# Optimization experiments

Measured on AMD Instinct MI355X. Metric: run time of the kernel, lower is better.

The kernel has to match this reference:

```python
import jax, jax.numpy as jnp
import numpy as np

BN_EPS = 1e-5


def _gin_layer(x, src, dst, W, b, num_nodes):
    # GINConv with eps=0: h_i = MLP(x_i + sum_{j in N(i)} x_j)
    agg = jax.ops.segment_sum(x[src], dst, num_segments=num_nodes)  # [N, F]
    h = (x + agg) @ W + b
    return jax.nn.relu(h)


def _batchnorm(h, gamma, beta):
    # training-mode BatchNorm1d: biased batch stats over the node dim
    mean = jnp.mean(h, axis=0)
    var = jnp.mean(jnp.square(h - mean), axis=0)
    return (h - mean) * jax.lax.rsqrt(var + BN_EPS) * gamma + beta


def setup_inputs() -> dict:
    key = jax.random.key(0)
    N, E, F, H = 50000, 800000, 128, 128
    ks = jax.random.split(key, 6)
    x = jax.random.normal(ks[0], (N, F), dtype=jnp.float32)
    edge_index = jax.random.randint(ks[1], (2, E), 0, N, dtype=jnp.int64)
    W1 = jax.random.normal(ks[2], (F, H), dtype=jnp.float32) * 0.05
    b1 = jnp.zeros((H,), dtype=jnp.float32)
    W2 = jax.random.normal(ks[3], (H, H), dtype=jnp.float32) * 0.05
    b2 = jnp.zeros((H,), dtype=jnp.float32)
    g1 = jnp.ones((H,), dtype=jnp.float32)
    be1 = jnp.zeros((H,), dtype=jnp.float32)
    g2 = jnp.ones((H,), dtype=jnp.float32)
    be2 = jnp.zeros((H,), dtype=jnp.float32)
    return {"x": x, "edge_index": edge_index, "W1": W1, "b1": b1,
            "W2": W2, "b2": b2, "g1": g1, "be1": be1, "g2": g2, "be2": be2}


def reference(x, edge_index, W1, b1, W2, b2, g1, be1, g2, be2):
    N = x.shape[0]
    src, dst = edge_index[0], edge_index[1]
    h = _gin_layer(x, src, dst, W1, b1, N)
    h = _batchnorm(h, g1, be1)
    h = _gin_layer(h, src, dst, W2, b2, N)
    return _batchnorm(h, g2, be2)
```

## Files before the change

### kernel.cpp

```cpp
#include <hip/hip_runtime.h>
#include <hip/hip_fp16.h>

#define FDIM 128
#define NGRP 8
#define CAP  64

typedef _Float16 half8_t __attribute__((ext_vector_type(8)));
typedef _Float16 half4_t __attribute__((ext_vector_type(4)));
typedef float float4_t __attribute__((ext_vector_type(4)));


__global__ void prep_kernel(int* __restrict__ zbase, int zn,
                            const float* __restrict__ x, _Float16* __restrict__ xh, int n4x,
                            const float* __restrict__ W1, _Float16* __restrict__ Wf1,
                            const float* __restrict__ W2, _Float16* __restrict__ Wf2,
                            int nzb, int ncb) {
  int b = blockIdx.x, t = threadIdx.x;
  if (b < nzb) {
    int i = b * 256 + t;
    if (i < zn) zbase[i] = 0;
  } else if (b < nzb + ncb) {
    int i = (b - nzb) * 256 + t;
    if (i < n4x) {
      float4 v = ((const float4*)x)[i];
      half4_t h;
      h.x = (_Float16)v.x; h.y = (_Float16)v.y; h.z = (_Float16)v.z; h.w = (_Float16)v.w;
      ((half4_t*)xh)[i] = h;
    }
  } else {
    int gid = (b - nzb - ncb) * 256 + t;
    int which = gid >> 14;
    int tid = gid & 16383;
    const float* W = which ? W2 : W1;
    _Float16* Wf = which ? Wf2 : Wf1;
    int j = tid & 7, lane = (tid >> 3) & 63, rest = tid >> 9;
    int kb = rest & 3, ct = (rest >> 2) & 1, wave = rest >> 3;
    int quad = lane >> 4, m16 = lane & 15;
    int k = kb * 32 + quad * 8 + j;
    int n = wave * 32 + ct * 16 + m16;
    Wf[tid] = (_Float16)W[k * FDIM + n];
  }
}


__global__ void place_part_kernel(const int* __restrict__ src, const int* __restrict__ dst,
                                  int* __restrict__ deg, int* __restrict__ ssrc,
                                  int E, int step) {
  int grp = blockIdx.x & (NGRP - 1);
  int nb = gridDim.x >> 3, bid = blockIdx.x >> 3;
  int lo = grp * step, hi = lo + step;
  int E4 = E >> 2;
  const int4* d4 = (const int4*)dst;
  const int4* s4 = (const int4*)src;
  for (int i = bid * blockDim.x + threadIdx.x; i < E4; i += nb * blockDim.x) {
    int4 d = d4[i];
    bool m0 = d.x >= lo && d.x < hi, m1 = d.y >= lo && d.y < hi;
    bool m2 = d.z >= lo && d.z < hi, m3 = d.w >= lo && d.w < hi;
    if (m0 | m1 | m2 | m3) {
      int4 s = s4[i];
      if (m0) { int p = atomicAdd(&deg[d.x], 1); if (p < CAP) ssrc[(d.x << 6) + p] = s.x; }
      if (m1) { int p = atomicAdd(&deg[d.y], 1); if (p < CAP) ssrc[(d.y << 6) + p] = s.y; }
      if (m2) { int p = atomicAdd(&deg[d.z], 1); if (p < CAP) ssrc[(d.z << 6) + p] = s.z; }
      if (m3) { int p = atomicAdd(&deg[d.w], 1); if (p < CAP) ssrc[(d.w << 6) + p] = s.w; }
    }
  }
  for (int e = (E4 << 2) + bid * blockDim.x + threadIdx.x; e < E; e += nb * blockDim.x) {
    int d = dst[e];
    if (d >= lo && d < hi) {
      int p = atomicAdd(&deg[d], 1);
      if (p < CAP) ssrc[(d << 6) + p] = src[e];
    }
  }
}


__device__ inline float2 up2(unsigned u) {
  __half2 h = *(__half2*)&u;
  return __half22float2(h);
}

__device__ inline void addrow(float* a, uint4 v) {
  float2 p0 = up2(v.x), p1 = up2(v.y), p2 = up2(v.z), p3 = up2(v.w);
  a[0] += p0.x; a[1] += p0.y; a[2] += p1.x; a[3] += p1.y;
  a[4] += p2.x; a[5] += p2.y; a[6] += p3.x; a[7] += p3.y;
}

template <bool SCALE>
__global__ void agg_kernel(const uint4* __restrict__ x4, const int* __restrict__ deg,
                           const int* __restrict__ ssrc, const float* __restrict__ a,
                           uint4* __restrict__ out4, int N) {
  int wave = (blockIdx.x * blockDim.x + threadIdx.x) >> 6;
  int lane = threadIdx.x & 63;
  if (wave >= N) return;
  int quad = lane >> 4, m16 = lane & 15;
  int d = deg[wave];
  if (d > CAP) d = CAP;
  int idx = ssrc[(wave << 6) + lane];

  float a0[8], a1[8];
  {
    uint4 v = x4[(size_t)wave * 16 + m16];
    float w0 = (quad == 0) ? 1.f : 0.f;
    float2 p0 = up2(v.x), p1 = up2(v.y), p2 = up2(v.z), p3 = up2(v.w);
    a0[0] = p0.x * w0; a0[1] = p0.y * w0; a0[2] = p1.x * w0; a0[3] = p1.y * w0;
    a0[4] = p2.x * w0; a0[5] = p2.y * w0; a0[6] = p3.x * w0; a0[7] = p3.y * w0;
#pragma unroll
    for (int j = 0; j < 8; j++) a1[j] = 0.f;
  }

  int d4 = d >> 2, tail = d & 3;
  int g = 0;
  for (; g + 3 < d4; g += 4) {
    int s0 = __shfl(idx, 4 * g + quad);
    int s1 = __shfl(idx, 4 * g + 4 + quad);
    int s2 = __shfl(idx, 4 * g + 8 + quad);
    int s3 = __shfl(idx, 4 * g + 12 + quad);
    uint4 v0 = x4[(size_t)s0 * 16 + m16];
    uint4 v1 = x4[(size_t)s1 * 16 + m16];
    uint4 v2 = x4[(size_t)s2 * 16 + m16];
    uint4 v3 = x4[(size_t)s3 * 16 + m16];
    addrow(a0, v0); addrow(a1, v1); addrow(a0, v2); addrow(a1, v3);
  }
  for (; g + 1 < d4; g += 2) {
    int s0 = __shfl(idx, 4 * g + quad);
    int s1 = __shfl(idx, 4 * g + 4 + quad);
    uint4 v0 = x4[(size_t)s0 * 16 + m16];
    uint4 v1 = x4[(size_t)s1 * 16 + m16];
    addrow(a0, v0); addrow(a1, v1);
  }
  if (g < d4) {
    int s0 = __shfl(idx, 4 * g + quad);
    uint4 v0 = x4[(size_t)s0 * 16 + m16];
    addrow(a0, v0);
  }
  if (tail) {
    int pos = 4 * d4 + quad;
    int s = __shfl(idx, pos);
    bool ok = quad < tail;
    int ss = ok ? s : wave;
    uint4 v = x4[(size_t)ss * 16 + m16];
    float w = ok ? 1.f : 0.f;
    float2 p0 = up2(v.x), p1 = up2(v.y), p2 = up2(v.z), p3 = up2(v.w);
    a1[0] += p0.x * w; a1[1] += p0.y * w; a1[2] += p1.x * w; a1[3] += p1.y * w;
    a1[4] += p2.x * w; a1[5] += p2.y * w; a1[6] += p3.x * w; a1[7] += p3.y * w;
  }

#pragma unroll
  for (int j = 0; j < 8; j++) a0[j] += a1[j];
#pragma unroll
  for (int j = 0; j < 8; j++) {
    a0[j] += __shfl_xor(a0[j], 16);
    a0[j] += __shfl_xor(a0[j], 32);
  }

  if (SCALE) {
    float4 av0 = ((const float4*)a)[2 * m16];
    float4 av1 = ((const float4*)a)[2 * m16 + 1];
    a0[0] *= av0.x; a0[1] *= av0.y; a0[2] *= av0.z; a0[3] *= av0.w;
    a0[4] *= av1.x; a0[5] *= av1.y; a0[6] *= av1.z; a0[7] *= av1.w;
  }

  if (quad == 0) {
    __half2 h0 = __floats2half2_rn(a0[0], a0[1]);
    __half2 h1 = __floats2half2_rn(a0[2], a0[3]);
    __half2 h2 = __floats2half2_rn(a0[4], a0[5]);
    __half2 h3 = __floats2half2_rn(a0[6], a0[7]);
    uint4 r;
    r.x = *(unsigned*)&h0; r.y = *(unsigned*)&h1;
    r.z = *(unsigned*)&h2; r.w = *(unsigned*)&h3;
    out4[(size_t)wave * 16 + m16] = r;
  }
}


template <bool LAYER2>
__global__ __launch_bounds__(256) void gemm_kernel(
    const _Float16* __restrict__ in, const _Float16* __restrict__ Wf,
    const float* __restrict__ bias, const float* __restrict__ r2,
    const int* __restrict__ deg, _Float16* __restrict__ outh,
    float* __restrict__ ssum, float* __restrict__ ssq,
    const float* __restrict__ gamma, const float* __restrict__ beta,
    const float* __restrict__ W2, float* __restrict__ aout, float* __restrict__ cout,
    int* __restrict__ counter, int N) {
  int t = threadIdx.x;
  int wave = t >> 6, lane = t & 63;
  int quad = lane >> 4, m16 = lane & 15;
  int row0 = blockIdx.x * 64;

  __shared__ float sdn[64];
  __shared__ float scc[FDIM];
  __shared__ int isLast;
  if (LAYER2) {
    if (t < 64) {
      int r = row0 + t;
      sdn[t] = (r < N) ? (float)(deg[r] + 1) : 0.f;
    }
    __syncthreads();
  }

  half8_t bf[2][4];
  const half8_t* wf8 = (const half8_t*)Wf;
#pragma unroll
  for (int ct = 0; ct < 2; ct++)
#pragma unroll
    for (int kb = 0; kb < 4; kb++)
      bf[ct][kb] = wf8[(size_t)(((wave * 2 + ct) * 4 + kb) * 64 + lane)];

  float4_t acc[4][2] = {};
#pragma unroll
  for (int rt = 0; rt < 4; rt++) {
    int arow = row0 + rt * 16 + m16;
    int cr = (arow < N) ? arow : N - 1;
#pragma unroll
    for (int kb = 0; kb < 4; kb++) {
      half8_t av = *(const half8_t*)(in + (size_t)cr * FDIM + kb * 32 + quad * 8);
      acc[rt][0] = __builtin_amdgcn_mfma_f32_16x16x32_f16(av, bf[0][kb], acc[rt][0], 0, 0, 0);
      acc[rt][1] = __builtin_amdgcn_mfma_f32_16x16x32_f16(av, bf[1][kb], acc[rt][1], 0, 0, 0);
    }
  }

#pragma unroll
  for (int ct = 0; ct < 2; ct++) {
    int col = wave * 32 + ct * 16 + m16;
    float bv = bias[col];
    float rv = LAYER2 ? r2[col] : 0.f;
    float s = 0.f, q = 0.f;
#pragma unroll
    for (int rt = 0; rt < 4; rt++) {
#pragma unroll
      for (int r = 0; r < 4; r++) {
        int row = row0 + rt * 16 + quad * 4 + r;
        if (row < N) {
          float v = acc[rt][ct][r] + bv;
          if (LAYER2) v += sdn[rt * 16 + quad * 4 + r] * rv;
          v = fmaxf(v, 0.f);
          outh[(size_t)row * FDIM + col] = (_Float16)v;
          s += v; q += v * v;
        }
      }
    }
    s += __shfl_xor(s, 16); q += __shfl_xor(q, 16);
    s += __shfl_xor(s, 32); q += __shfl_xor(q, 32);
    if (quad == 0) {
      atomicAdd(&ssum[col], s);
      atomicAdd(&ssq[col], q);
    }
  }

  __syncthreads();
  if (t == 0) {
    int v = atomicAdd(counter, 1);
    isLast = (v == (int)gridDim.x - 1);
  }
  __syncthreads();
  if (!isLast) return;

  if (t < FDIM) {
    float sm = atomicAdd(&ssum[t], 0.f);
    float qv = atomicAdd(&ssq[t], 0.f);
    float invn = 1.f / (float)N;
    float mean = sm * invn;
    float var = qv * invn - mean * mean;
    float rs = rsqrtf(var + 1e-5f);
    float av = gamma[t] * rs;
    aout[t] = av;
    float cv = beta[t] - mean * av;
    if (LAYER2) cout[t] = cv;
    else scc[t] = cv;
  }
  if (!LAYER2) {
    __syncthreads();
    if (t < FDIM) {
      float acc2 = 0.f;
      for (int k = 0; k < FDIM; k++) acc2 += scc[k] * W2[k * FDIM + t];
      cout[t] = acc2;
    }
  }
}


__global__ void apply_h_kernel(const uint2* __restrict__ h4, const float* __restrict__ a,
                               const float* __restrict__ c, float4* __restrict__ out, int n4) {
  int i = blockIdx.x * blockDim.x + threadIdx.x;
  if (i < n4) {
    uint2 u = h4[i];
    float2 v0 = up2(u.x), v1 = up2(u.y);
    int c4 = i & 31;
    float4 av = ((const float4*)a)[c4];
    float4 cv = ((const float4*)c)[c4];
    float4 o;
    o.x = av.x * v0.x + cv.x;
    o.y = av.y * v0.y + cv.y;
    o.z = av.z * v1.x + cv.z;
    o.w = av.w * v1.y + cv.w;
    out[i] = o;
  }
}


extern "C" void kernel_launch(void* const* d_in, const int* in_sizes, int n_in,
                              void* d_out, int out_size, void* d_ws, size_t ws_size,
                              hipStream_t stream) {
  const float* x   = (const float*)d_in[0];
  const int*   ei  = (const int*)d_in[1];
  const float* W1  = (const float*)d_in[2];
  const float* b1  = (const float*)d_in[3];
  const float* W2  = (const float*)d_in[4];
  const float* b2  = (const float*)d_in[5];
  const float* g1  = (const float*)d_in[6];
  const float* be1 = (const float*)d_in[7];
  const float* g2  = (const float*)d_in[8];
  const float* be2 = (const float*)d_in[9];
  float* out = (float*)d_out;

  const int N = in_sizes[0] / FDIM;
  const int E = in_sizes[1] / 2;
  const int* src = ei;
  const int* dst = ei + E;

  auto align256 = [](char*& q) { q = (char*)(((uintptr_t)q + 255) & ~(uintptr_t)255); };

  char* p = (char*)d_ws;
  int* deg = (int*)p;        p += (size_t)N * 4;
  float* stats = (float*)p;  p += 1280 * 4;
  align256(p);
  int* ssrc = (int*)p;       p += (size_t)N * CAP * 4; align256(p);
  _Float16* xh  = (_Float16*)p; p += (size_t)N * FDIM * 2; align256(p);
  _Float16* h1  = (_Float16*)p; p += (size_t)N * FDIM * 2; align256(p);
  _Float16* h2  = (_Float16*)p; p += (size_t)N * FDIM * 2; align256(p);
  _Float16* Wf1 = (_Float16*)p; p += FDIM * FDIM * 2;
  _Float16* Wf2 = (_Float16*)p; p += FDIM * FDIM * 2;

  float* s1 = stats + 0,   *q1 = stats + 128;
  float* s2 = stats + 256, *q2 = stats + 384;
  float* a1 = stats + 512, *r2 = stats + 640;
  float* a2 = stats + 768, *c2 = stats + 896;
  int* cnt1 = (int*)(stats + 1024);
  int* cnt2 = (int*)(stats + 1088);

  const int ntiles = (N + 63) / 64;
  const int step = (N + NGRP - 1) / NGRP;

  const int zn = N + 1280;
  const int nzb = (zn + 255) / 256;
  const int n4x = N * 32;
  const int ncb = (n4x + 255) / 256;

  prep_kernel<<<nzb + ncb + 128, 256, 0, stream>>>((int*)deg, zn, x, xh, n4x,
                                                   W1, Wf1, W2, Wf2, nzb, ncb);
  place_part_kernel<<<NGRP * 128, 256, 0, stream>>>(src, dst, deg, ssrc, E, step);

  agg_kernel<false><<<(N + 3) / 4, 256, 0, stream>>>((const uint4*)xh, deg, ssrc,
                                                     nullptr, (uint4*)h2, N);
  gemm_kernel<false><<<ntiles, 256, 0, stream>>>(h2, Wf1, b1, nullptr, nullptr, h1,
                                                 s1, q1, g1, be1, W2, a1, r2, cnt1, N);

  agg_kernel<true><<<(N + 3) / 4, 256, 0, stream>>>((const uint4*)h1, deg, ssrc,
                                                    a1, (uint4*)xh, N);
  gemm_kernel<true><<<ntiles, 256, 0, stream>>>(xh, Wf2, b2, r2, deg, h2,
                                                s2, q2, g2, be2, nullptr, a2, c2, cnt2, N);

  int n4 = N * 32;
  apply_h_kernel<<<(n4 + 255) / 256, 256, 0, stream>>>((const uint2*)h2, a2, c2,
                                                       (float4*)out, n4);
}
```

Measured before the change: 262.2 us.

## Fuse neighbor aggregation into GEMM kernel via swizzled LDS tile

Merges the gather-sum aggregation kernel into the MFMA GEMM kernel for each layer. Each block aggregates its 64 rows (16 per wave, serially) into a 16 KB XOR-swizzled shared-memory tile, then feeds the MFMA directly from LDS. This removes one kernel launch per layer and the global write and read of the aggregated fp16 intermediate. In exchange the grid shrinks from about 12.5k blocks to about 780, and each wave handles 16 nodes in sequence, so there is less parallelism for hiding gather latency. The extra LDS per block may also limit occupancy.

```diff
diff --git a/kernel.cpp b/kernel.cpp
--- a/kernel.cpp
+++ b/kernel.cpp
@@ -85,99 +85,12 @@
   a[4] += p2.x; a[5] += p2.y; a[6] += p3.x; a[7] += p3.y;
 }
 
-template <bool SCALE>
-__global__ void agg_kernel(const uint4* __restrict__ x4, const int* __restrict__ deg,
-                           const int* __restrict__ ssrc, const float* __restrict__ a,
-                           uint4* __restrict__ out4, int N) {
-  int wave = (blockIdx.x * blockDim.x + threadIdx.x) >> 6;
-  int lane = threadIdx.x & 63;
-  if (wave >= N) return;
-  int quad = lane >> 4, m16 = lane & 15;
-  int d = deg[wave];
-  if (d > CAP) d = CAP;
-  int idx = ssrc[(wave << 6) + lane];
-
-  float a0[8], a1[8];
-  {
-    uint4 v = x4[(size_t)wave * 16 + m16];
-    float w0 = (quad == 0) ? 1.f : 0.f;
-    float2 p0 = up2(v.x), p1 = up2(v.y), p2 = up2(v.z), p3 = up2(v.w);
-    a0[0] = p0.x * w0; a0[1] = p0.y * w0; a0[2] = p1.x * w0; a0[3] = p1.y * w0;
-    a0[4] = p2.x * w0; a0[5] = p2.y * w0; a0[6] = p3.x * w0; a0[7] = p3.y * w0;
-#pragma unroll
-    for (int j = 0; j < 8; j++) a1[j] = 0.f;
-  }
-
-  int d4 = d >> 2, tail = d & 3;
-  int g = 0;
-  for (; g + 3 < d4; g += 4) {
-    int s0 = __shfl(idx, 4 * g + quad);
-    int s1 = __shfl(idx, 4 * g + 4 + quad);
-    int s2 = __shfl(idx, 4 * g + 8 + quad);
-    int s3 = __shfl(idx, 4 * g + 12 + quad);
-    uint4 v0 = x4[(size_t)s0 * 16 + m16];
-    uint4 v1 = x4[(size_t)s1 * 16 + m16];
-    uint4 v2 = x4[(size_t)s2 * 16 + m16];
-    uint4 v3 = x4[(size_t)s3 * 16 + m16];
-    addrow(a0, v0); addrow(a1, v1); addrow(a0, v2); addrow(a1, v3);
-  }
-  for (; g + 1 < d4; g += 2) {
-    int s0 = __shfl(idx, 4 * g + quad);
-    int s1 = __shfl(idx, 4 * g + 4 + quad);
-    uint4 v0 = x4[(size_t)s0 * 16 + m16];
-    uint4 v1 = x4[(size_t)s1 * 16 + m16];
-    addrow(a0, v0); addrow(a1, v1);
-  }
-  if (g < d4) {
-    int s0 = __shfl(idx, 4 * g + quad);
-    uint4 v0 = x4[(size_t)s0 * 16 + m16];
-    addrow(a0, v0);
-  }
-  if (tail) {
-    int pos = 4 * d4 + quad;
-    int s = __shfl(idx, pos);
-    bool ok = quad < tail;
-    int ss = ok ? s : wave;
-    uint4 v = x4[(size_t)ss * 16 + m16];
-    float w = ok ? 1.f : 0.f;
-    float2 p0 = up2(v.x), p1 = up2(v.y), p2 = up2(v.z), p3 = up2(v.w);
-    a1[0] += p0.x * w; a1[1] += p0.y * w; a1[2] += p1.x * w; a1[3] += p1.y * w;
-    a1[4] += p2.x * w; a1[5] += p2.y * w; a1[6] += p3.x * w; a1[7] += p3.y * w;
-  }
-
-#pragma unroll
-  for (int j = 0; j < 8; j++) a0[j] += a1[j];
-#pragma unroll
-  for (int j = 0; j < 8; j++) {
-    a0[j] += __shfl_xor(a0[j], 16);
-    a0[j] += __shfl_xor(a0[j], 32);
-  }
-
-  if (SCALE) {
-    float4 av0 = ((const float4*)a)[2 * m16];
-    float4 av1 = ((const float4*)a)[2 * m16 + 1];
-    a0[0] *= av0.x; a0[1] *= av0.y; a0[2] *= av0.z; a0[3] *= av0.w;
-    a0[4] *= av1.x; a0[5] *= av1.y; a0[6] *= av1.z; a0[7] *= av1.w;
-  }
-
-  if (quad == 0) {
-    __half2 h0 = __floats2half2_rn(a0[0], a0[1]);
-    __half2 h1 = __floats2half2_rn(a0[2], a0[3]);
-    __half2 h2 = __floats2half2_rn(a0[4], a0[5]);
-    __half2 h3 = __floats2half2_rn(a0[6], a0[7]);
-    uint4 r;
-    r.x = *(unsigned*)&h0; r.y = *(unsigned*)&h1;
-    r.z = *(unsigned*)&h2; r.w = *(unsigned*)&h3;
-    out4[(size_t)wave * 16 + m16] = r;
-  }
-}
-
-
 template <bool LAYER2>
-__global__ __launch_bounds__(256) void gemm_kernel(
-    const _Float16* __restrict__ in, const _Float16* __restrict__ Wf,
-    const float* __restrict__ bias, const float* __restrict__ r2,
-    const int* __restrict__ deg, _Float16* __restrict__ outh,
+__global__ __launch_bounds__(256) void fused_kernel(
+    const uint4* __restrict__ x4, const int* __restrict__ deg,
+    const int* __restrict__ ssrc, const float* __restrict__ ascale,
+    const _Float16* __restrict__ Wf, const float* __restrict__ bias,
+    const float* __restrict__ r2v, _Float16* __restrict__ outh,
     float* __restrict__ ssum, float* __restrict__ ssq,
     const float* __restrict__ gamma, const float* __restrict__ beta,
     const float* __restrict__ W2, float* __restrict__ aout, float* __restrict__ cout,
@@ -187,16 +100,104 @@
   int quad = lane >> 4, m16 = lane & 15;
   int row0 = blockIdx.x * 64;
 
+  __shared__ __align__(16) unsigned char sAb[64 * 256];
   __shared__ float sdn[64];
   __shared__ float scc[FDIM];
   __shared__ int isLast;
-  if (LAYER2) {
-    if (t < 64) {
-      int r = row0 + t;
-      sdn[t] = (r < N) ? (float)(deg[r] + 1) : 0.f;
-    }
+
+  if (LAYER2 && t < 64) {
+    int r = row0 + t;
+    sdn[t] = (r < N) ? (float)(deg[r] + 1) : 0.f;
+  }
+
+  if (row0 + 64 > N) {
+    for (int j = t; j < 64 * 16; j += 256) ((uint4*)sAb)[j] = make_uint4(0u, 0u, 0u, 0u);
     __syncthreads();
   }
+
+  for (int i = 0; i < 16; i++) {
+    int ln = wave * 16 + i;
+    int node = row0 + ln;
+    if (node >= N) break;
+    int d = deg[node];
+    if (d > CAP) d = CAP;
+    int idx = ssrc[(node << 6) + lane];
+
+    float a0[8], a1[8];
+    {
+      uint4 v = x4[(size_t)node * 16 + m16];
+      float w0 = (quad == 0) ? 1.f : 0.f;
+      float2 p0 = up2(v.x), p1 = up2(v.y), p2 = up2(v.z), p3 = up2(v.w);
+      a0[0] = p0.x * w0; a0[1] = p0.y * w0; a0[2] = p1.x * w0; a0[3] = p1.y * w0;
+      a0[4] = p2.x * w0; a0[5] = p2.y * w0; a0[6] = p3.x * w0; a0[7] = p3.y * w0;
+#pragma unroll
+      for (int j = 0; j < 8; j++) a1[j] = 0.f;
+    }
+
+    int d4 = d >> 2, tail = d & 3;
+    int g = 0;
+    for (; g + 3 < d4; g += 4) {
+      int s0 = __shfl(idx, 4 * g + quad);
+      int s1 = __shfl(idx, 4 * g + 4 + quad);
+      int s2 = __shfl(idx, 4 * g + 8 + quad);
+      int s3 = __shfl(idx, 4 * g + 12 + quad);
+      uint4 v0 = x4[(size_t)s0 * 16 + m16];
+      uint4 v1 = x4[(size_t)s1 * 16 + m16];
+      uint4 v2 = x4[(size_t)s2 * 16 + m16];
+      uint4 v3 = x4[(size_t)s3 * 16 + m16];
+      addrow(a0, v0); addrow(a1, v1); addrow(a0, v2); addrow(a1, v3);
+    }
+    for (; g + 1 < d4; g += 2) {
+      int s0 = __shfl(idx, 4 * g + quad);
+      int s1 = __shfl(idx, 4 * g + 4 + quad);
+      uint4 v0 = x4[(size_t)s0 * 16 + m16];
+      uint4 v1 = x4[(size_t)s1 * 16 + m16];
+      addrow(a0, v0); addrow(a1, v1);
+    }
+    if (g < d4) {
+      int s0 = __shfl(idx, 4 * g + quad);
+      uint4 v0 = x4[(size_t)s0 * 16 + m16];
+      addrow(a0, v0);
+    }
+    if (tail) {
+      int pos = 4 * d4 + quad;
+      int s = __shfl(idx, pos);
+      bool ok = quad < tail;
+      int ss = ok ? s : node;
+      uint4 v = x4[(size_t)ss * 16 + m16];
+      float w = ok ? 1.f : 0.f;
+      float2 p0 = up2(v.x), p1 = up2(v.y), p2 = up2(v.z), p3 = up2(v.w);
+      a1[0] += p0.x * w; a1[1] += p0.y * w; a1[2] += p1.x * w; a1[3] += p1.y * w;
+      a1[4] += p2.x * w; a1[5] += p2.y * w; a1[6] += p3.x * w; a1[7] += p3.y * w;
+    }
+
+#pragma unroll
+    for (int j = 0; j < 8; j++) a0[j] += a1[j];
+#pragma unroll
+    for (int j = 0; j < 8; j++) {
+      a0[j] += __shfl_xor(a0[j], 16);
+      a0[j] += __shfl_xor(a0[j], 32);
+    }
+
+    if (LAYER2) {
+      float4 av0 = ((const float4*)ascale)[2 * m16];
+      float4 av1 = ((const float4*)ascale)[2 * m16 + 1];
+      a0[0] *= av0.x; a0[1] *= av0.y; a0[2] *= av0.z; a0[3] *= av0.w;
+      a0[4] *= av1.x; a0[5] *= av1.y; a0[6] *= av1.z; a0[7] *= av1.w;
+    }
+
+    if (quad == 0) {
+      __half2 h0 = __floats2half2_rn(a0[0], a0[1]);
+      __half2 h1 = __floats2half2_rn(a0[2], a0[3]);
+      __half2 h2 = __floats2half2_rn(a0[4], a0[5]);
+      __half2 h3 = __floats2half2_rn(a0[6], a0[7]);
+      uint4 r;
+      r.x = *(unsigned*)&h0; r.y = *(unsigned*)&h1;
+      r.z = *(unsigned*)&h2; r.w = *(unsigned*)&h3;
+      *(uint4*)(sAb + ln * 256 + ((m16 * 16) ^ ((ln & 7) << 4))) = r;
+    }
+  }
+  __syncthreads();
 
   half8_t bf[2][4];
   const half8_t* wf8 = (const half8_t*)Wf;
@@ -209,11 +210,11 @@
   float4_t acc[4][2] = {};
 #pragma unroll
   for (int rt = 0; rt < 4; rt++) {
-    int arow = row0 + rt * 16 + m16;
-    int cr = (arow < N) ? arow : N - 1;
+    int arow = rt * 16 + m16;
 #pragma unroll
     for (int kb = 0; kb < 4; kb++) {
-      half8_t av = *(const half8_t*)(in + (size_t)cr * FDIM + kb * 32 + quad * 8);
+      half8_t av = *(const half8_t*)(sAb + arow * 256 +
+                                     ((kb * 64 + quad * 16) ^ ((arow & 7) << 4)));
       acc[rt][0] = __builtin_amdgcn_mfma_f32_16x16x32_f16(av, bf[0][kb], acc[rt][0], 0, 0, 0);
       acc[rt][1] = __builtin_amdgcn_mfma_f32_16x16x32_f16(av, bf[1][kb], acc[rt][1], 0, 0, 0);
     }
@@ -223,7 +224,7 @@
   for (int ct = 0; ct < 2; ct++) {
     int col = wave * 32 + ct * 16 + m16;
     float bv = bias[col];
-    float rv = LAYER2 ? r2[col] : 0.f;
+    float rv = LAYER2 ? r2v[col] : 0.f;
     float s = 0.f, q = 0.f;
 #pragma unroll
     for (int rt = 0; rt < 4; rt++) {
@@ -350,15 +351,13 @@
                                                    W1, Wf1, W2, Wf2, nzb, ncb);
   place_part_kernel<<<NGRP * 128, 256, 0, stream>>>(src, dst, deg, ssrc, E, step);
 
-  agg_kernel<false><<<(N + 3) / 4, 256, 0, stream>>>((const uint4*)xh, deg, ssrc,
-                                                     nullptr, (uint4*)h2, N);
-  gemm_kernel<false><<<ntiles, 256, 0, stream>>>(h2, Wf1, b1, nullptr, nullptr, h1,
-                                                 s1, q1, g1, be1, W2, a1, r2, cnt1, N);
-
-  agg_kernel<true><<<(N + 3) / 4, 256, 0, stream>>>((const uint4*)h1, deg, ssrc,
-                                                    a1, (uint4*)xh, N);
-  gemm_kernel<true><<<ntiles, 256, 0, stream>>>(xh, Wf2, b2, r2, deg, h2,
-                                                s2, q2, g2, be2, nullptr, a2, c2, cnt2, N);
+  fused_kernel<false><<<ntiles, 256, 0, stream>>>((const uint4*)xh, deg, ssrc, nullptr,
+                                                  Wf1, b1, nullptr, h1, s1, q1,
+                                                  g1, be1, W2, a1, r2, cnt1, N);
+
+  fused_kernel<true><<<ntiles, 256, 0, stream>>>((const uint4*)h1, deg, ssrc, a1,
+                                                 Wf2, b2, r2, h2, s2, q2,
+                                                 g2, be2, nullptr, a2, c2, cnt2, N);
 
   int n4 = N * 32;
   apply_h_kernel<<<(n4 + 255) / 256, 256, 0, stream>>>((const uint2*)h2, a2, c2,
```

Result: no change. 259.8 us (-0.9%).
